# Performance work log

Measured on AMD Instinct MI355X. Metric: run time of the kernel, lower is better.

The kernel has to match this reference:

```python
import jax, jax.numpy as jnp
import numpy as np

N, E, F, H, G, C = 50000, 800000, 128, 64, 512, 10
RATIO = 0.5  # forward arg `ratio` baked as constant


def seg_mean(msgs, idx, n):
    s = jax.ops.segment_sum(msgs, idx, num_segments=n)
    cnt = jax.ops.segment_sum(jnp.ones(idx.shape[0], msgs.dtype), idx, num_segments=n)
    return s / jnp.maximum(cnt, 1.0)[:, None]


def sage(x, src, dst, Wl, bl, Wr, ew=None):
    # PyG SAGEConv: lin_l(mean_{j->i} msg_j) + lin_r(x_i); weighted variant scales messages
    m = x[src] if ew is None else x[src] * ew[:, None]
    agg = seg_mean(m, dst, x.shape[0])
    return agg @ Wl + bl + x @ Wr


def topk_mask(scores, seg, num_graphs, ratio):
    # per-graph (segment) top-k edge selection: keep ceil(ratio*edges_in_graph) highest scores
    e = scores.shape[0]
    counts = jax.ops.segment_sum(jnp.ones(e, jnp.float32), seg, num_segments=num_graphs)
    order = jnp.lexsort((-scores, seg))  # sort by segment, then score descending
    seg_sorted = seg[order]
    starts = jnp.concatenate([jnp.zeros(1, jnp.float32), jnp.cumsum(counts)[:-1]])
    rank = jnp.arange(e, dtype=jnp.float32) - starts[seg_sorted]
    k = jnp.ceil(ratio * counts)
    sel = (rank < k[seg_sorted]).astype(scores.dtype)
    return jnp.zeros(e, scores.dtype).at[order].set(sel)


def setup_inputs():
    key = jax.random.key(0)
    ks = jax.random.split(key, 16)
    w = lambda k, shape, fan: (jax.random.normal(k, shape, jnp.float32) / np.sqrt(fan))
    return {
        'x': jax.random.normal(ks[0], (N, F), jnp.float32),
        'edge_index': jax.random.randint(ks[1], (2, E), 0, N, jnp.int32),
        'batch': jnp.sort(jax.random.randint(ks[2], (N,), 0, G, jnp.int32)),
        'W1l': w(ks[3], (F, H), F), 'b1l': jnp.zeros(H, jnp.float32), 'W1r': w(ks[4], (F, H), F),
        'W2l': w(ks[5], (H, H), H), 'b2l': jnp.zeros(H, jnp.float32), 'W2r': w(ks[6], (H, H), H),
        'W3l': w(ks[7], (H, H), H), 'b3l': jnp.zeros(H, jnp.float32), 'W3r': w(ks[8], (H, H), H),
        'Wlin1': w(ks[9], (H, H), H), 'blin1': jnp.zeros(H, jnp.float32),
        'Wlin2': w(ks[10], (H, C), H), 'blin2': jnp.zeros(C, jnp.float32),
    }


def reference(x, edge_index, batch, W1l, b1l, W1r, W2l, b2l, W2r, W3l, b3l, W3r, Wlin1, blin1, Wlin2, blin2):
    src, dst = edge_index[0], edge_index[1]
    h = jax.nn.relu(sage(x, src, dst, W1l, b1l, W1r))
    edge_scores = jnp.sum(h[src] * h[dst], axis=-1)  # [E]
    seg = batch[src]  # graph id per edge (sections)
    sampled = topk_mask(edge_scores, seg, G, RATIO)
    ew = edge_scores * sampled
    h = jax.nn.relu(sage(h, src, dst, W2l, b2l, W2r, ew))
    h = jax.nn.relu(sage(h, src, dst, W3l, b3l, W3r, ew))
    pooled = seg_mean(h, batch, G)  # global_mean_pool
    z = jax.nn.relu(pooled @ Wlin1 + blin1)
    z = z @ Wlin2 + blin2  # dropout inactive in eval
    return jax.nn.log_softmax(z, axis=-1), sampled
```

## Files before the change

### kernel.cpp

```cpp
#include <hip/hip_runtime.h>
#include <hip/hip_bf16.h>
#include <math.h>

static constexpr int N = 50000;
static constexpr int E = 800000;
static constexpr int F = 128;
static constexpr int H = 64;
static constexpr int G = 512;
static constexpr int C = 10;
static constexpr int CAP = 256;
static constexpr int NWIN = 8;
static constexpr int EB = E / 256;
static constexpr int GB2 = (N + 31) / 32;
static constexpr int SB = E / 256;

static inline int cdiv(long a, int b) { return (int)((a + b - 1) / b); }

__device__ __forceinline__ float uinv_score(unsigned u) {
  return (u & 0x80000000u) ? __uint_as_float(u & 0x7fffffffu) : __uint_as_float(~u);
}

__device__ __forceinline__ int2 pack_slot(int s, int d, int g, int e) {
  unsigned a = (unsigned)s | ((unsigned)(d & 0x7FFF) << 17);
  unsigned b = ((unsigned)d >> 15) | ((unsigned)g << 2) | ((unsigned)e << 11);
  return make_int2((int)a, (int)b);
}
__device__ __forceinline__ int slot_src(int2 p) { return p.x & 0x1FFFF; }
__device__ __forceinline__ int slot_dst(int2 p) {
  return (int)(((unsigned)p.x >> 17) | (((unsigned)p.y & 3u) << 15));
}
__device__ __forceinline__ int slot_g(int2 p) { return (int)(((unsigned)p.y >> 2) & 0x1FFu); }
__device__ __forceinline__ int slot_eid(int2 p) { return (int)((unsigned)p.y >> 11); }

__global__ void k_deg_goff(const int* __restrict__ dst, const int* __restrict__ batch,
                           int* __restrict__ deg, int* __restrict__ goff) {
  for (int i = blockIdx.x * 256 + threadIdx.x; i < N; i += gridDim.x * 256) {
    int b = batch[i];
    if (i == 0) {
      for (int g = 0; g <= b; ++g) goff[g] = 0;
    } else {
      int p = batch[i - 1];
      for (int g = p + 1; g <= b; ++g) goff[g] = i;
    }
    if (i == N - 1) {
      for (int g = b + 1; g <= G; ++g) goff[g] = N;
    }
  }
  const int4* d4 = (const int4*)dst;
  for (int i = blockIdx.x * 256 + threadIdx.x; i < E / 4; i += gridDim.x * 256) {
    int4 v = d4[i];
    atomicAdd(&deg[v.x], 1);
    atomicAdd(&deg[v.y], 1);
    atomicAdd(&deg[v.z], 1);
    atomicAdd(&deg[v.w], 1);
  }
}

__global__ void k_scan_a(const int* __restrict__ cnt, int* __restrict__ off,
                         int* __restrict__ bsum, int n) {
  __shared__ int wsum[16];
  int tid = threadIdx.x, lane = tid & 63, wv = tid >> 6;
  int idx = blockIdx.x * 4096 + tid * 4;
  int v0 = (idx + 0 < n) ? cnt[idx + 0] : 0;
  int v1 = (idx + 1 < n) ? cnt[idx + 1] : 0;
  int v2 = (idx + 2 < n) ? cnt[idx + 2] : 0;
  int v3 = (idx + 3 < n) ? cnt[idx + 3] : 0;
  int local = v0 + v1 + v2 + v3;
  int inc = local;
  for (int d = 1; d < 64; d <<= 1) {
    int t = __shfl_up(inc, d);
    if (lane >= d) inc += t;
  }
  if (lane == 63) wsum[wv] = inc;
  __syncthreads();
  if (tid < 16) {
    int t = wsum[tid];
    for (int d = 1; d < 16; d <<= 1) {
      int u = __shfl_up(t, d);
      if (tid >= d) t += u;
    }
    wsum[tid] = t;
  }
  __syncthreads();
  int woff = (wv > 0) ? wsum[wv - 1] : 0;
  int excl = woff + inc - local;
  if (idx + 0 < n) off[idx + 0] = excl;
  if (idx + 1 < n) off[idx + 1] = excl + v0;
  if (idx + 2 < n) off[idx + 2] = excl + v0 + v1;
  if (idx + 3 < n) off[idx + 3] = excl + v0 + v1 + v2;
  if (tid == 0) bsum[blockIdx.x] = wsum[15];
}

__global__ void k_scan_c(int* __restrict__ off, int* __restrict__ cursor,
                         const int* __restrict__ bsum, int n, int nb) {
  __shared__ int spre[34];
  int tid = threadIdx.x;
  if (tid < 32) {
    int v = (tid < nb) ? bsum[tid] : 0;
    int inc = v;
    for (int d = 1; d < 32; d <<= 1) {
      int t = __shfl_up(inc, d);
      if (tid >= d) inc += t;
    }
    spre[tid] = inc - v;
  }
  __syncthreads();
  int i = blockIdx.x * 256 + tid;
  if (i < n) {
    int v = off[i] + spre[i >> 12];
    off[i] = v;
    cursor[i] = v;
  } else if (i == n) {
    off[n] = spre[nb];
  }
}

__global__ void k_fill_gemm(const int* __restrict__ src, const int* __restrict__ dst,
                            const int* __restrict__ batch, int* __restrict__ cursor,
                            int2* __restrict__ csrp, int* __restrict__ einv,
                            const float* __restrict__ x, const float* __restrict__ Wl,
                            const float* __restrict__ Wr, const float* __restrict__ bl,
                            float* __restrict__ y, float* __restrict__ r) {
  __shared__ float sx[16][F];
  int lane = threadIdx.x, ty = threadIdx.y;
  int bq = blockIdx.x / 9, br = blockIdx.x - bq * 9;
  if (br == 0) {
    int tid = ty * 64 + lane;
    int row0 = bq * 16;
    const float4* gsrc = (const float4*)(x + (size_t)row0 * F);
    float4* sdst = (float4*)(&sx[0][0]);
#pragma unroll
    for (int i = tid; i < 16 * F / 4; i += 256) sdst[i] = gsrc[i];
    __syncthreads();
    float al[4], ar[4];
    float bias = bl[lane];
#pragma unroll
    for (int j = 0; j < 4; ++j) { al[j] = 0.f; ar[j] = bias; }
#pragma unroll 4
    for (int f = 0; f < F; ++f) {
      float wl = Wl[f * H + lane];
      float wr = Wr[f * H + lane];
#pragma unroll
      for (int j = 0; j < 4; ++j) {
        float xv = sx[ty * 4 + j][f];
        al[j] += xv * wl;
        ar[j] += xv * wr;
      }
    }
#pragma unroll
    for (int j = 0; j < 4; ++j) {
      int row = row0 + ty * 4 + j;
      y[(size_t)row * H + lane] = al[j];
      r[(size_t)row * H + lane] = ar[j];
    }
  } else {
    int tid = ty * 64 + lane;
    int fid = bq * 8 + (br - 1);
    int win = fid / EB;
    int blk = fid - win * EB;
    int e = blk * 256 + tid;
    int d = dst[e];
    int lo = win * (N / NWIN), hi = lo + (N / NWIN);
    if (d < lo || d >= hi) return;
    int s = src[e];
    int g = batch[s];
    int slot = atomicAdd(&cursor[d], 1);
    csrp[slot] = pack_slot(s, d, g, e);
    einv[e] = slot;
  }
}

template <int K>
__global__ void k_gemm2h(const float* __restrict__ in, const float* __restrict__ Wl,
                         const float* __restrict__ Wr, const float* __restrict__ b,
                         __hip_bfloat16* __restrict__ y, float* __restrict__ r) {
  __shared__ float sx[16][K];
  int lane = threadIdx.x, ty = threadIdx.y;
  int tid = ty * 64 + lane;
  int row0 = blockIdx.x * 16;
  const float4* gsrc = (const float4*)(in + (size_t)row0 * K);
  float4* sdst = (float4*)(&sx[0][0]);
#pragma unroll
  for (int i = tid; i < 16 * K / 4; i += 256) sdst[i] = gsrc[i];
  __syncthreads();
  float al[4], ar[4];
  float bias = b[lane];
#pragma unroll
  for (int j = 0; j < 4; ++j) { al[j] = 0.f; ar[j] = bias; }
#pragma unroll 4
  for (int f = 0; f < K; ++f) {
    float wl = Wl[f * H + lane];
    float wr = Wr[f * H + lane];
#pragma unroll
    for (int j = 0; j < 4; ++j) {
      float xv = sx[ty * 4 + j][f];
      al[j] += xv * wl;
      ar[j] += xv * wr;
    }
  }
#pragma unroll
  for (int j = 0; j < 4; ++j) {
    int row = row0 + ty * 4 + j;
    y[(size_t)row * H + lane] = __float2bfloat16(al[j]);
    r[(size_t)row * H + lane] = ar[j];
  }
}

__global__ void k_agg1(const float* __restrict__ y, const float* __restrict__ r,
                       const int2* __restrict__ csrp, const int* __restrict__ off,
                       float* __restrict__ out) {
  int node = blockIdx.x * 8 + threadIdx.y;
  int lane = threadIdx.x;
  int q = lane >> 3, c = lane & 7;
  int s0 = off[node], s1 = off[node + 1];
  float4 a0 = make_float4(0.f, 0.f, 0.f, 0.f);
  float4 a1 = make_float4(0.f, 0.f, 0.f, 0.f);
  int i = s0 + q;
  for (; i + 8 < s1; i += 16) {
    int se0 = slot_src(csrp[i]);
    int se1 = slot_src(csrp[i + 8]);
    const float4* p0 = (const float4*)(y + (size_t)se0 * H);
    const float4* p1 = (const float4*)(y + (size_t)se1 * H);
    float4 u0 = p0[c], v0 = p0[c + 8];
    float4 u1 = p1[c], v1 = p1[c + 8];
    a0.x += u0.x + u1.x; a0.y += u0.y + u1.y; a0.z += u0.z + u1.z; a0.w += u0.w + u1.w;
    a1.x += v0.x + v1.x; a1.y += v0.y + v1.y; a1.z += v0.z + v1.z; a1.w += v0.w + v1.w;
  }
  for (; i < s1; i += 8) {
    int se = slot_src(csrp[i]);
    const float4* p = (const float4*)(y + (size_t)se * H);
    float4 u = p[c], v = p[c + 8];
    a0.x += u.x; a0.y += u.y; a0.z += u.z; a0.w += u.w;
    a1.x += v.x; a1.y += v.y; a1.z += v.z; a1.w += v.w;
  }
#pragma unroll
  for (int d = 8; d < 64; d <<= 1) {
    a0.x += __shfl_xor(a0.x, d); a0.y += __shfl_xor(a0.y, d);
    a0.z += __shfl_xor(a0.z, d); a0.w += __shfl_xor(a0.w, d);
    a1.x += __shfl_xor(a1.x, d); a1.y += __shfl_xor(a1.y, d);
    a1.z += __shfl_xor(a1.z, d); a1.w += __shfl_xor(a1.w, d);
  }
  if (q == 0) {
    float inv = 1.f / fmaxf((float)(s1 - s0), 1.f);
    const float4* rp = (const float4*)(r + (size_t)node * H);
    float4 r0 = rp[c], r1 = rp[c + 8];
    float4 o0, o1;
    o0.x = fmaxf(a0.x * inv + r0.x, 0.f); o0.y = fmaxf(a0.y * inv + r0.y, 0.f);
    o0.z = fmaxf(a0.z * inv + r0.z, 0.f); o0.w = fmaxf(a0.w * inv + r0.w, 0.f);
    o1.x = fmaxf(a1.x * inv + r1.x, 0.f); o1.y = fmaxf(a1.y * inv + r1.y, 0.f);
    o1.z = fmaxf(a1.z * inv + r1.z, 0.f); o1.w = fmaxf(a1.w * inv + r1.w, 0.f);
    float4* op = (float4*)(out + (size_t)node * H);
    op[c] = o0; op[c + 8] = o1;
  }
}

__global__ void k_agg_w(const __hip_bfloat16* __restrict__ y, const float* __restrict__ r,
                        const int2* __restrict__ csr2, const int* __restrict__ cnt2,
                        const int* __restrict__ off, float* __restrict__ out) {
  int node = blockIdx.x * 8 + threadIdx.y;
  int lane = threadIdx.x;
  int q = lane >> 3, c = lane & 7;
  int b0 = off[node], cn = cnt2[node];
  float a[8] = {0.f, 0.f, 0.f, 0.f, 0.f, 0.f, 0.f, 0.f};
  for (int j = q; j < cn; j += 8) {
    int2 sw = csr2[b0 + j];
    float w = __int_as_float(sw.y);
    uint4 pk = ((const uint4*)((const unsigned short*)y + (size_t)sw.x * H))[c];
    a[0] += w * __uint_as_float(pk.x << 16); a[1] += w * __uint_as_float(pk.x & 0xffff0000u);
    a[2] += w * __uint_as_float(pk.y << 16); a[3] += w * __uint_as_float(pk.y & 0xffff0000u);
    a[4] += w * __uint_as_float(pk.z << 16); a[5] += w * __uint_as_float(pk.z & 0xffff0000u);
    a[6] += w * __uint_as_float(pk.w << 16); a[7] += w * __uint_as_float(pk.w & 0xffff0000u);
  }
#pragma unroll
  for (int d = 8; d < 64; d <<= 1) {
#pragma unroll
    for (int j = 0; j < 8; ++j) a[j] += __shfl_xor(a[j], d);
  }
  if (q == 0) {
    int degn = off[node + 1] - off[node];
    float inv = 1.f / fmaxf((float)degn, 1.f);
    const float4* rp = (const float4*)(r + (size_t)node * H);
    float4 r0 = rp[2 * c], r1 = rp[2 * c + 1];
    float4 o0, o1;
    o0.x = fmaxf(a[0] * inv + r0.x, 0.f); o0.y = fmaxf(a[1] * inv + r0.y, 0.f);
    o0.z = fmaxf(a[2] * inv + r0.z, 0.f); o0.w = fmaxf(a[3] * inv + r0.w, 0.f);
    o1.x = fmaxf(a[4] * inv + r1.x, 0.f); o1.y = fmaxf(a[5] * inv + r1.y, 0.f);
    o1.z = fmaxf(a[6] * inv + r1.z, 0.f); o1.w = fmaxf(a[7] * inv + r1.w, 0.f);
    float4* op = (float4*)(out + (size_t)node * H);
    op[2 * c] = o0; op[2 * c + 1] = o1;
  }
}

__global__ void k_score_g2h(const float* __restrict__ h1, const int2* __restrict__ csrp,
                            unsigned* __restrict__ scoreu_csr,
                            unsigned short* __restrict__ seg_csr, int* __restrict__ hist,
                            const float* __restrict__ Wl, const float* __restrict__ Wr,
                            const float* __restrict__ bl,
                            __hip_bfloat16* __restrict__ y, float* __restrict__ r) {
  __shared__ float sx[32][H];
  int lane = threadIdx.x, ty = threadIdx.y;
  int q3 = blockIdx.x / 3, r3 = blockIdx.x - q3 * 3;
  if (r3 == 0 && q3 < GB2) {
    int tid = ty * 64 + lane;
    int row0 = q3 * 32;
    {
      int row = row0 + (tid >> 4);
      if (row < N)
        ((float4*)(&sx[0][0]))[tid] = ((const float4*)h1)[(size_t)row * (H / 4) + (tid & 15)];
    }
    __syncthreads();
    float al[4], ar[4];
    float bias = bl[lane];
#pragma unroll
    for (int j = 0; j < 4; ++j) { al[j] = 0.f; ar[j] = bias; }
#pragma unroll 4
    for (int f = 0; f < H; ++f) {
      float wl = Wl[f * H + lane];
      float wr = Wr[f * H + lane];
#pragma unroll
      for (int j = 0; j < 4; ++j) {
        float xv = sx[ty * 4 + j][f];
        al[j] += xv * wl;
        ar[j] += xv * wr;
      }
    }
#pragma unroll
    for (int j = 0; j < 4; ++j) {
      int row = row0 + ty * 4 + j;
      if (row < N) {
        y[(size_t)row * H + lane] = __float2bfloat16(al[j]);
        r[(size_t)row * H + lane] = ar[j];
      }
    }
  } else {
    int sid = blockIdx.x - (q3 + (r3 > 0 ? 1 : 0));
    int q = lane >> 4, c = lane & 15;
    int s = (sid * 8 + ty) * 32 + q * 8;
    int2 se[8];
#pragma unroll
    for (int j = 0; j < 8; ++j) se[j] = csrp[s + j];
    float4 xr[8], yr[8];
#pragma unroll
    for (int j = 0; j < 8; ++j)
      xr[j] = ((const float4*)(h1 + (size_t)slot_src(se[j]) * H))[c];
#pragma unroll
    for (int j = 0; j < 8; ++j)
      yr[j] = ((const float4*)(h1 + (size_t)slot_dst(se[j]) * H))[c];
    float p[8];
#pragma unroll
    for (int j = 0; j < 8; ++j)
      p[j] = yr[j].x * xr[j].x + yr[j].y * xr[j].y + yr[j].z * xr[j].z + yr[j].w * xr[j].w;
#pragma unroll
    for (int d = 1; d < 16; d <<= 1) {
#pragma unroll
      for (int j = 0; j < 8; ++j) p[j] += __shfl_xor(p[j], d);
    }
    if (c == 0) {
#pragma unroll
      for (int j = 0; j < 8; ++j) {
        int g = slot_g(se[j]);
        unsigned u = __float_as_uint(p[j]);
        u = (u & 0x80000000u) ? ~u : (u | 0x80000000u);
        scoreu_csr[s + j] = u;
        seg_csr[s + j] = (unsigned short)g;
        atomicAdd(&hist[g * 256 + (int)(u >> 24)], 1);
      }
    }
  }
}

__global__ void k_hist(const unsigned* __restrict__ scoreu, const unsigned short* __restrict__ seg,
                       const unsigned* __restrict__ prefix, int* __restrict__ hist, int pass) {
  int e = (blockIdx.x * 256 + threadIdx.x) * 4;
  if (e >= E) return;
  uint4 u4 = *(const uint4*)(scoreu + e);
  ushort4 s4 = *(const ushort4*)(seg + e);
  unsigned uu[4] = {u4.x, u4.y, u4.z, u4.w};
  int gg[4] = {(int)s4.x, (int)s4.y, (int)s4.z, (int)s4.w};
  int predshift = 32 - 8 * pass;
  int bshift = 24 - 8 * pass;
#pragma unroll
  for (int j = 0; j < 4; ++j) {
    unsigned u = uu[j];
    int g = gg[j];
    if ((u >> predshift) == (prefix[g] >> predshift))
      atomicAdd(&hist[g * 256 + (int)((u >> bshift) & 0xFFu)], 1);
  }
}

__global__ void k_scan(int* __restrict__ hist, unsigned* __restrict__ prefix,
                       int* __restrict__ krem, int pass) {
  int g = blockIdx.x;
  int lane = threadIdx.x;
  int4* row = (int4*)(hist + (size_t)g * 256);
  int4 v = row[lane];
  int vj[4] = {v.x, v.y, v.z, v.w};
  int s = v.x + v.y + v.z + v.w;
  int inc = s;
  for (int d = 1; d < 64; d <<= 1) {
    int t = __shfl_up(inc, d);
    if (lane >= d) inc += t;
  }
  int T = __shfl(inc, 63);
  int k = (pass == 0) ? ((T + 1) >> 1) : krem[g];
  int excl = inc - s;
  int pre[4] = {excl, excl + vj[0], excl + vj[0] + vj[1], excl + vj[0] + vj[1] + vj[2]};
  int bsel_l = -1, newk_l = 0;
  if (k > 0) {
    for (int j = 3; j >= 0; --j) {
      int suf = T - pre[j];
      if (suf >= k) { bsel_l = 4 * lane + j; newk_l = k - (suf - vj[j]); break; }
    }
  }
  unsigned long long mask = __ballot(bsel_l >= 0);
  int bsel = 255, newk = 0;
  if (k > 0 && mask) {
    int hi = 63 - __builtin_clzll(mask);
    bsel = __shfl(bsel_l, hi);
    newk = __shfl(newk_l, hi);
  }
  if (lane == 0) {
    unsigned base = (pass == 0) ? 0u : prefix[g];
    prefix[g] = base | ((unsigned)bsel << (24 - 8 * pass));
    krem[g] = newk;
  }
  row[lane] = make_int4(0, 0, 0, 0);
}

__global__ void k_select(const unsigned* __restrict__ scoreu_csr,
                         const unsigned short* __restrict__ seg_csr,
                         const unsigned* __restrict__ thresh,
                         int* __restrict__ eqcnt, int* __restrict__ eqlist,
                         unsigned char* __restrict__ sel_csr, float* __restrict__ ew_csr) {
  int s = (blockIdx.x * 256 + threadIdx.x) * 4;
  if (s >= E) return;
  uint4 u4 = *(const uint4*)(scoreu_csr + s);
  ushort4 g4 = *(const ushort4*)(seg_csr + s);
  unsigned uu[4] = {u4.x, u4.y, u4.z, u4.w};
  int gg[4] = {(int)g4.x, (int)g4.y, (int)g4.z, (int)g4.w};
  float ew[4];
  unsigned char sl[4];
#pragma unroll
  for (int j = 0; j < 4; ++j) {
    unsigned u = uu[j];
    int g = gg[j];
    unsigned t = thresh[g];
    unsigned um = u & 0xffffff00u;
    float sel = 0.f;
    if (um > t) sel = 1.f;
    else if (um == t) {
      int slot = atomicAdd(&eqcnt[g], 1);
      if (slot < CAP) eqlist[g * CAP + slot] = s + j;
    }
    sl[j] = (unsigned char)sel;
    ew[j] = uinv_score(u) * sel;
  }
  *(uchar4*)(sel_csr + s) = make_uchar4(sl[0], sl[1], sl[2], sl[3]);
  *(float4*)(ew_csr + s) = make_float4(ew[0], ew[1], ew[2], ew[3]);
}

__global__ void k_resolve(const int* __restrict__ krem, const int* __restrict__ eqcnt,
                          const int* __restrict__ eqlist, const int2* __restrict__ csrp,
                          const unsigned* __restrict__ scoreu_csr,
                          unsigned char* __restrict__ sel_csr, float* __restrict__ ew_csr) {
  int g = blockIdx.x * 256 + threadIdx.x;
  if (g >= G) return;
  int c = eqcnt[g]; if (c > CAP) c = CAP;
  int r = krem[g];  if (r > c) r = c;
  const int* lst = eqlist + g * CAP;
  unsigned last_u = 0u; int last_e = -1; bool first = true;
  for (int i = 0; i < r; ++i) {
    unsigned bu = 0u; int be = -1, bs = -1;
    for (int j = 0; j < c; ++j) {
      int slot = lst[j];
      unsigned u = scoreu_csr[slot];
      int eid = slot_eid(csrp[slot]);
      bool after = first || (u < last_u) || (u == last_u && eid > last_e);
      if (after && (bs < 0 || u > bu || (u == bu && eid < be))) { bu = u; be = eid; bs = slot; }
    }
    if (bs < 0) break;
    sel_csr[bs] = 1;
    ew_csr[bs] = uinv_score(bu);
    last_u = bu; last_e = be; first = false;
  }
}

__global__ void k_samp_comp(const unsigned char* __restrict__ sel,
                            const int2* __restrict__ csrp, const float* __restrict__ ewc,
                            const int* __restrict__ off, int2* __restrict__ csr2,
                            int* __restrict__ cnt2,
                            const int* __restrict__ einv, float* __restrict__ sampled) {
  int lane = threadIdx.x, ty = threadIdx.y;
  if (blockIdx.x < N / 8) {
    int node = blockIdx.x * 8 + ty;
    int s0 = off[node], s1 = off[node + 1];
    unsigned long long lt = ((unsigned long long)1 << lane) - 1;
    int cum = 0;
    for (int i0 = s0; i0 < s1; i0 += 64) {
      int i = i0 + lane;
      bool f = (i < s1) && sel[i];
      unsigned long long m = __ballot(f);
      if (f) {
        int rank = __popcll(m & lt);
        csr2[s0 + cum + rank] = make_int2(slot_src(csrp[i]), __float_as_int(ewc[i]));
      }
      cum += __popcll(m);
    }
    if (lane == 0) cnt2[node] = cum;
  } else {
    int tid = ty * 64 + lane;
    int e = ((blockIdx.x - N / 8) * 512 + tid) * 4;
    if (e >= E) return;
    int4 iv = *(const int4*)(einv + e);
    float4 o;
    o.x = (float)sel[iv.x];
    o.y = (float)sel[iv.y];
    o.z = (float)sel[iv.z];
    o.w = (float)sel[iv.w];
    *(float4*)(sampled + e) = o;
  }
}

__global__ void k_poolhead(const float* __restrict__ h3, const int* __restrict__ goff,
                           const float* __restrict__ W1, const float* __restrict__ b1,
                           const float* __restrict__ W2, const float* __restrict__ b2,
                           float* __restrict__ outp) {
  int g = blockIdx.x;
  int tid = threadIdx.x;
  int h = tid & 63, j = tid >> 6;
  int s0 = goff[g], s1 = goff[g + 1];
  float a = 0.f;
  for (int n = s0 + j; n < s1; n += 8) a += h3[(size_t)n * H + h];
  __shared__ float sp[8][H];
  __shared__ float p[H], z1[H], z2[C];
  __shared__ float lse;
  sp[j][h] = a;
  __syncthreads();
  if (j == 0) {
    float s = sp[0][h] + sp[1][h] + sp[2][h] + sp[3][h]
            + sp[4][h] + sp[5][h] + sp[6][h] + sp[7][h];
    float inv = 1.f / fmaxf((float)(s1 - s0), 1.f);
    p[h] = s * inv;
  }
  __syncthreads();
  if (j == 0) {
    float acc = b1[h];
#pragma unroll 8
    for (int f = 0; f < H; ++f) acc += p[f] * W1[f * H + h];
    z1[h] = fmaxf(acc, 0.f);
  }
  __syncthreads();
  if (tid < C) {
    float a2 = b2[tid];
#pragma unroll 8
    for (int f = 0; f < H; ++f) a2 += z1[f] * W2[f * C + tid];
    z2[tid] = a2;
  }
  __syncthreads();
  if (tid == 0) {
    float m = z2[0];
    for (int c = 1; c < C; ++c) m = fmaxf(m, z2[c]);
    float s = 0.f;
    for (int c = 0; c < C; ++c) s += expf(z2[c] - m);
    lse = m + logf(s);
  }
  __syncthreads();
  if (tid < C) outp[(size_t)g * C + tid] = z2[tid] - lse;
}

extern "C" void kernel_launch(void* const* d_in, const int* in_sizes, int n_in,
                              void* d_out, int out_size, void* d_ws, size_t ws_size,
                              hipStream_t stream) {
  const float* x     = (const float*)d_in[0];
  const int*   ei    = (const int*)d_in[1];
  const int*   batch = (const int*)d_in[2];
  const float* W1l   = (const float*)d_in[3];
  const float* b1l   = (const float*)d_in[4];
  const float* W1r   = (const float*)d_in[5];
  const float* W2l   = (const float*)d_in[6];
  const float* b2l   = (const float*)d_in[7];
  const float* W2r   = (const float*)d_in[8];
  const float* W3l   = (const float*)d_in[9];
  const float* b3l   = (const float*)d_in[10];
  const float* W3r   = (const float*)d_in[11];
  const float* Wlin1 = (const float*)d_in[12];
  const float* blin1 = (const float*)d_in[13];
  const float* Wlin2 = (const float*)d_in[14];
  const float* blin2 = (const float*)d_in[15];

  const int* srcv = ei;
  const int* dstv = ei + E;

  float* out_ls   = (float*)d_out;
  float* out_samp = out_ls + G * C;

  char* w = (char*)d_ws;
  auto carve = [&](size_t bytes) { void* p = (void*)w; w += (bytes + 255) & ~(size_t)255; return p; };
  char* zbase   = w;
  int*      deg     = (int*)carve((size_t)N * 4);
  int*      eqcnt   = (int*)carve((size_t)G * 4);
  int*      hist    = (int*)carve((size_t)G * 256 * 4);
  size_t    zbytes  = (size_t)(w - zbase);
  float*    h1      = (float*)carve((size_t)N * H * 4);
  float*    h2      = (float*)carve((size_t)N * H * 4);
  float*    h3      = (float*)carve((size_t)N * H * 4);
  float*    yb      = (float*)carve((size_t)N * H * 4);
  float*    rb      = (float*)carve((size_t)N * H * 4);
  __hip_bfloat16* ybh = (__hip_bfloat16*)carve((size_t)N * H * 2);
  unsigned* scoreu_csr = (unsigned*)carve((size_t)E * 4);
  unsigned short* seg_csr = (unsigned short*)carve((size_t)E * 2);
  float*    ew_csr     = (float*)carve((size_t)E * 4);
  unsigned char* sel_csr = (unsigned char*)carve((size_t)E);
  int2*     csrp    = (int2*)carve((size_t)E * 8);
  int*      einv    = (int*)carve((size_t)E * 4);
  int*      off     = (int*)carve((size_t)(N + 1) * 4);
  int*      cursor  = (int*)carve((size_t)N * 4);
  int*      cnt2    = (int*)carve((size_t)N * 4);
  int*      goff    = (int*)carve((size_t)(G + 1) * 4);
  unsigned* prefix  = (unsigned*)carve((size_t)G * 4);
  int*      krem    = (int*)carve((size_t)G * 4);
  int*      eqlist  = (int*)carve((size_t)G * CAP * 4);
  int*      bsum    = (int*)carve((size_t)16 * 4);
  int2*     csr2    = (int2*)carve((size_t)E * 8);

  hipMemsetAsync(zbase, 0, zbytes, stream);

  k_deg_goff<<<256, 256, 0, stream>>>(dstv, batch, deg, goff);
  int nb = cdiv(N, 4096);
  k_scan_a<<<nb, 1024, 0, stream>>>(deg, off, bsum, N);
  k_scan_c<<<cdiv(N + 1, 256), 256, 0, stream>>>(off, cursor, bsum, N, nb);

  k_fill_gemm<<<9 * EB, dim3(64, 4), 0, stream>>>(srcv, dstv, batch, cursor, csrp, einv,
                                                  x, W1l, W1r, b1l, yb, rb);

  k_agg1<<<N / 8, dim3(64, 8), 0, stream>>>(yb, rb, csrp, off, h1);

  k_score_g2h<<<SB + GB2, dim3(64, 8), 0, stream>>>(h1, csrp, scoreu_csr, seg_csr, hist,
                                                    W2l, W2r, b2l, ybh, rb);
  k_scan<<<G, 64, 0, stream>>>(hist, prefix, krem, 0);
  for (int p = 1; p <= 2; ++p) {
    k_hist<<<cdiv(E / 4, 256), 256, 0, stream>>>(scoreu_csr, seg_csr, prefix, hist, p);
    k_scan<<<G, 64, 0, stream>>>(hist, prefix, krem, p);
  }
  k_select<<<cdiv(E / 4, 256), 256, 0, stream>>>(scoreu_csr, seg_csr, prefix,
                                                 eqcnt, eqlist, sel_csr, ew_csr);
  k_resolve<<<cdiv(G, 256), 256, 0, stream>>>(krem, eqcnt, eqlist, csrp, scoreu_csr,
                                              sel_csr, ew_csr);

  k_samp_comp<<<N / 8 + cdiv(E / 4, 512), dim3(64, 8), 0, stream>>>(
      sel_csr, csrp, ew_csr, off, csr2, cnt2, einv, out_samp);

  k_agg_w<<<N / 8, dim3(64, 8), 0, stream>>>(ybh, rb, csr2, cnt2, off, h2);

  k_gemm2h<H><<<N / 16, dim3(64, 4), 0, stream>>>(h2, W3l, W3r, b3l, ybh, rb);
  k_agg_w<<<N / 8, dim3(64, 8), 0, stream>>>(ybh, rb, csr2, cnt2, off, h3);

  k_poolhead<<<G, 512, 0, stream>>>(h3, goff, Wlin1, blin1, Wlin2, blin2, out_ls);
}
```

Baseline: 424.0 us.

## Move layer-1 GEMM into degree kernel and batch CSR fill per window

The first-layer dense projection moves out of the CSR fill kernel and into the degree/graph-offset kernel as extra blocks, so it overlaps the atomic degree counting instead of the fill phase. The fill kernel becomes standalone. Each block now handles a 1280-edge chunk for one destination window and preloads the dst values into registers before the atomic slot assignment. This cuts the block count and the scheduling overhead of the old 9-way interleaved launch, but the GEMM blocks now compete with the degree atomics, and the larger per-block work may reduce parallelism. Two shuffle statements are also swapped, which has no effect.

```diff
diff --git a/kernel.cpp b/kernel.cpp
--- a/kernel.cpp
+++ b/kernel.cpp
@@ -10,7 +10,9 @@
 static constexpr int C = 10;
 static constexpr int CAP = 256;
 static constexpr int NWIN = 8;
-static constexpr int EB = E / 256;
+static constexpr int FILL_CH = 1280;
+static constexpr int FB = E / FILL_CH;
+static constexpr int DEGB = 256;
 static constexpr int GB2 = (N + 31) / 32;
 static constexpr int SB = E / 256;
 
@@ -32,9 +34,45 @@
 __device__ __forceinline__ int slot_g(int2 p) { return (int)(((unsigned)p.y >> 2) & 0x1FFu); }
 __device__ __forceinline__ int slot_eid(int2 p) { return (int)((unsigned)p.y >> 11); }
 
-__global__ void k_deg_goff(const int* __restrict__ dst, const int* __restrict__ batch,
-                           int* __restrict__ deg, int* __restrict__ goff) {
-  for (int i = blockIdx.x * 256 + threadIdx.x; i < N; i += gridDim.x * 256) {
+__global__ void k_deg_gemm(const int* __restrict__ dst, const int* __restrict__ batch,
+                           int* __restrict__ deg, int* __restrict__ goff,
+                           const float* __restrict__ x, const float* __restrict__ Wl,
+                           const float* __restrict__ Wr, const float* __restrict__ bl,
+                           float* __restrict__ y, float* __restrict__ r) {
+  __shared__ float sx[16][F];
+  int lane = threadIdx.x, ty = threadIdx.y;
+  int tid = ty * 64 + lane;
+  if (blockIdx.x >= DEGB) {
+    int row0 = (blockIdx.x - DEGB) * 16;
+    const float4* gsrc = (const float4*)(x + (size_t)row0 * F);
+    float4* sdst = (float4*)(&sx[0][0]);
+#pragma unroll
+    for (int i = tid; i < 16 * F / 4; i += 256) sdst[i] = gsrc[i];
+    __syncthreads();
+    float al[4], ar[4];
+    float bias = bl[lane];
+#pragma unroll
+    for (int j = 0; j < 4; ++j) { al[j] = 0.f; ar[j] = bias; }
+#pragma unroll 4
+    for (int f = 0; f < F; ++f) {
+      float wl = Wl[f * H + lane];
+      float wr = Wr[f * H + lane];
+#pragma unroll
+      for (int j = 0; j < 4; ++j) {
+        float xv = sx[ty * 4 + j][f];
+        al[j] += xv * wl;
+        ar[j] += xv * wr;
+      }
+    }
+#pragma unroll
+    for (int j = 0; j < 4; ++j) {
+      int row = row0 + ty * 4 + j;
+      y[(size_t)row * H + lane] = al[j];
+      r[(size_t)row * H + lane] = ar[j];
+    }
+    return;
+  }
+  for (int i = blockIdx.x * 256 + tid; i < N; i += DEGB * 256) {
     int b = batch[i];
     if (i == 0) {
       for (int g = 0; g <= b; ++g) goff[g] = 0;
@@ -47,7 +85,7 @@
     }
   }
   const int4* d4 = (const int4*)dst;
-  for (int i = blockIdx.x * 256 + threadIdx.x; i < E / 4; i += gridDim.x * 256) {
+  for (int i = blockIdx.x * 256 + tid; i < E / 4; i += DEGB * 256) {
     int4 v = d4[i];
     atomicAdd(&deg[v.x], 1);
     atomicAdd(&deg[v.y], 1);
@@ -115,58 +153,27 @@
   }
 }
 
-__global__ void k_fill_gemm(const int* __restrict__ src, const int* __restrict__ dst,
-                            const int* __restrict__ batch, int* __restrict__ cursor,
-                            int2* __restrict__ csrp, int* __restrict__ einv,
-                            const float* __restrict__ x, const float* __restrict__ Wl,
-                            const float* __restrict__ Wr, const float* __restrict__ bl,
-                            float* __restrict__ y, float* __restrict__ r) {
-  __shared__ float sx[16][F];
-  int lane = threadIdx.x, ty = threadIdx.y;
-  int bq = blockIdx.x / 9, br = blockIdx.x - bq * 9;
-  if (br == 0) {
-    int tid = ty * 64 + lane;
-    int row0 = bq * 16;
-    const float4* gsrc = (const float4*)(x + (size_t)row0 * F);
-    float4* sdst = (float4*)(&sx[0][0]);
-#pragma unroll
-    for (int i = tid; i < 16 * F / 4; i += 256) sdst[i] = gsrc[i];
-    __syncthreads();
-    float al[4], ar[4];
-    float bias = bl[lane];
-#pragma unroll
-    for (int j = 0; j < 4; ++j) { al[j] = 0.f; ar[j] = bias; }
-#pragma unroll 4
-    for (int f = 0; f < F; ++f) {
-      float wl = Wl[f * H + lane];
-      float wr = Wr[f * H + lane];
-#pragma unroll
-      for (int j = 0; j < 4; ++j) {
-        float xv = sx[ty * 4 + j][f];
-        al[j] += xv * wl;
-        ar[j] += xv * wr;
-      }
-    }
-#pragma unroll
-    for (int j = 0; j < 4; ++j) {
-      int row = row0 + ty * 4 + j;
-      y[(size_t)row * H + lane] = al[j];
-      r[(size_t)row * H + lane] = ar[j];
-    }
-  } else {
-    int tid = ty * 64 + lane;
-    int fid = bq * 8 + (br - 1);
-    int win = fid / EB;
-    int blk = fid - win * EB;
-    int e = blk * 256 + tid;
-    int d = dst[e];
-    int lo = win * (N / NWIN), hi = lo + (N / NWIN);
-    if (d < lo || d >= hi) return;
-    int s = src[e];
-    int g = batch[s];
-    int slot = atomicAdd(&cursor[d], 1);
-    csrp[slot] = pack_slot(s, d, g, e);
-    einv[e] = slot;
+__global__ void k_fill(const int* __restrict__ src, const int* __restrict__ dst,
+                       const int* __restrict__ batch, int* __restrict__ cursor,
+                       int2* __restrict__ csrp, int* __restrict__ einv) {
+  int win = blockIdx.x & 7;
+  int chunk = blockIdx.x >> 3;
+  int lo = win * (N / NWIN), hi = lo + (N / NWIN);
+  int base = chunk * FILL_CH + threadIdx.x;
+  int dd[FILL_CH / 256];
+#pragma unroll
+  for (int it = 0; it < FILL_CH / 256; ++it) dd[it] = dst[base + it * 256];
+#pragma unroll
+  for (int it = 0; it < FILL_CH / 256; ++it) {
+    int d = dd[it];
+    if (d >= lo && d < hi) {
+      int e = base + it * 256;
+      int s = src[e];
+      int g = batch[s];
+      int slot = atomicAdd(&cursor[d], 1);
+      csrp[slot] = pack_slot(s, d, g, e);
+      einv[e] = slot;
+    }
   }
 }
 
@@ -238,7 +245,7 @@
     a0.x += __shfl_xor(a0.x, d); a0.y += __shfl_xor(a0.y, d);
     a0.z += __shfl_xor(a0.z, d); a0.w += __shfl_xor(a0.w, d);
     a1.x += __shfl_xor(a1.x, d); a1.y += __shfl_xor(a1.y, d);
-    a1.z += __shfl_xor(a1.z, d); a1.w += __shfl_xor(a1.w, d);
+    a1.w += __shfl_xor(a1.w, d); a1.z += __shfl_xor(a1.z, d);
   }
   if (q == 0) {
     float inv = 1.f / fmaxf((float)(s1 - s0), 1.f);
@@ -625,13 +632,13 @@
 
   hipMemsetAsync(zbase, 0, zbytes, stream);
 
-  k_deg_goff<<<256, 256, 0, stream>>>(dstv, batch, deg, goff);
+  k_deg_gemm<<<DEGB + N / 16, dim3(64, 4), 0, stream>>>(dstv, batch, deg, goff,
+                                                        x, W1l, W1r, b1l, yb, rb);
   int nb = cdiv(N, 4096);
   k_scan_a<<<nb, 1024, 0, stream>>>(deg, off, bsum, N);
   k_scan_c<<<cdiv(N + 1, 256), 256, 0, stream>>>(off, cursor, bsum, N, nb);
 
-  k_fill_gemm<<<9 * EB, dim3(64, 4), 0, stream>>>(srcv, dstv, batch, cursor, csrp, einv,
-                                                  x, W1l, W1r, b1l, yb, rb);
+  k_fill<<<8 * FB, 256, 0, stream>>>(srcv, dstv, batch, cursor, csrp, einv);
 
   k_agg1<<<N / 8, dim3(64, 8), 0, stream>>>(yb, rb, csrp, off, h1);
 
```

New measurement: 436.9 us. 1.03x slower.

## Reuse degree-count atomic return values as CSR ranks to avoid second atomic pass

Applied to the files above, without the earlier changes.

The return value of the degree-counting atomicAdd is stored as a per-edge 16-bit rank. The CSR fill then computes each slot as off[dst]+rank with no atomics. This removes the 8-window filtered fill pass and the cursor array, and each fill thread now handles four edges with vectorised loads. The cost is an extra E*2-byte buffer written and read. Ordering within a row still depends on atomic order, and ranks are truncated to 16 bits, which assumes node in-degree stays below 65536.

```diff
diff --git a/kernel.cpp b/kernel.cpp
--- a/kernel.cpp
+++ b/kernel.cpp
@@ -9,8 +9,8 @@
 static constexpr int G = 512;
 static constexpr int C = 10;
 static constexpr int CAP = 256;
-static constexpr int NWIN = 8;
-static constexpr int EB = E / 256;
+static constexpr int NFB = (E / 4 + 255) / 256;
+static constexpr int GB1 = N / 16;
 static constexpr int GB2 = (N + 31) / 32;
 static constexpr int SB = E / 256;
 
@@ -33,8 +33,10 @@
 __device__ __forceinline__ int slot_eid(int2 p) { return (int)((unsigned)p.y >> 11); }
 
 __global__ void k_deg_goff(const int* __restrict__ dst, const int* __restrict__ batch,
-                           int* __restrict__ deg, int* __restrict__ goff) {
-  for (int i = blockIdx.x * 256 + threadIdx.x; i < N; i += gridDim.x * 256) {
+                           int* __restrict__ deg, int* __restrict__ goff,
+                           unsigned short* __restrict__ rank16) {
+  int tid = threadIdx.x;
+  for (int i = blockIdx.x * 256 + tid; i < N; i += gridDim.x * 256) {
     int b = batch[i];
     if (i == 0) {
       for (int g = 0; g <= b; ++g) goff[g] = 0;
@@ -47,12 +49,14 @@
     }
   }
   const int4* d4 = (const int4*)dst;
-  for (int i = blockIdx.x * 256 + threadIdx.x; i < E / 4; i += gridDim.x * 256) {
+  for (int i = blockIdx.x * 256 + tid; i < E / 4; i += gridDim.x * 256) {
     int4 v = d4[i];
-    atomicAdd(&deg[v.x], 1);
-    atomicAdd(&deg[v.y], 1);
-    atomicAdd(&deg[v.z], 1);
-    atomicAdd(&deg[v.w], 1);
+    ushort4 rk;
+    rk.x = (unsigned short)atomicAdd(&deg[v.x], 1);
+    rk.y = (unsigned short)atomicAdd(&deg[v.y], 1);
+    rk.z = (unsigned short)atomicAdd(&deg[v.z], 1);
+    rk.w = (unsigned short)atomicAdd(&deg[v.w], 1);
+    *(ushort4*)(rank16 + (size_t)i * 4) = rk;
   }
 }
 
@@ -91,8 +95,7 @@
   if (tid == 0) bsum[blockIdx.x] = wsum[15];
 }
 
-__global__ void k_scan_c(int* __restrict__ off, int* __restrict__ cursor,
-                         const int* __restrict__ bsum, int n, int nb) {
+__global__ void k_scan_c(int* __restrict__ off, const int* __restrict__ bsum, int n, int nb) {
   __shared__ int spre[34];
   int tid = threadIdx.x;
   if (tid < 32) {
@@ -107,66 +110,73 @@
   __syncthreads();
   int i = blockIdx.x * 256 + tid;
   if (i < n) {
-    int v = off[i] + spre[i >> 12];
-    off[i] = v;
-    cursor[i] = v;
+    off[i] = off[i] + spre[i >> 12];
   } else if (i == n) {
     off[n] = spre[nb];
   }
 }
 
 __global__ void k_fill_gemm(const int* __restrict__ src, const int* __restrict__ dst,
-                            const int* __restrict__ batch, int* __restrict__ cursor,
+                            const unsigned short* __restrict__ rank16,
+                            const int* __restrict__ batch, const int* __restrict__ off,
                             int2* __restrict__ csrp, int* __restrict__ einv,
                             const float* __restrict__ x, const float* __restrict__ Wl,
                             const float* __restrict__ Wr, const float* __restrict__ bl,
                             float* __restrict__ y, float* __restrict__ r) {
   __shared__ float sx[16][F];
   int lane = threadIdx.x, ty = threadIdx.y;
-  int bq = blockIdx.x / 9, br = blockIdx.x - bq * 9;
+  int tid = ty * 64 + lane;
+  int bq = blockIdx.x / 5, br = blockIdx.x - bq * 5;
   if (br == 0) {
-    int tid = ty * 64 + lane;
-    int row0 = bq * 16;
-    const float4* gsrc = (const float4*)(x + (size_t)row0 * F);
-    float4* sdst = (float4*)(&sx[0][0]);
-#pragma unroll
-    for (int i = tid; i < 16 * F / 4; i += 256) sdst[i] = gsrc[i];
-    __syncthreads();
-    float al[4], ar[4];
-    float bias = bl[lane];
-#pragma unroll
-    for (int j = 0; j < 4; ++j) { al[j] = 0.f; ar[j] = bias; }
+    int i = bq * 256 + tid;
+    if (i < E / 4) {
+      int4 dv = ((const int4*)dst)[i];
+      int4 sv = ((const int4*)src)[i];
+      ushort4 rv = *(const ushort4*)(rank16 + (size_t)i * 4);
+      int dd[4] = {dv.x, dv.y, dv.z, dv.w};
+      int ss[4] = {sv.x, sv.y, sv.z, sv.w};
+      int rr[4] = {rv.x, rv.y, rv.z, rv.w};
+      int e0 = i * 4;
+      int slots[4];
+#pragma unroll
+      for (int j = 0; j < 4; ++j) {
+        int g = batch[ss[j]];
+        int slot = off[dd[j]] + rr[j];
+        csrp[slot] = pack_slot(ss[j], dd[j], g, e0 + j);
+        slots[j] = slot;
+      }
+      *(int4*)(einv + e0) = make_int4(slots[0], slots[1], slots[2], slots[3]);
+    }
+    return;
+  }
+  int gid = bq * 4 + (br - 1);
+  if (gid >= GB1) return;
+  int row0 = gid * 16;
+  const float4* gsrc = (const float4*)(x + (size_t)row0 * F);
+  float4* sdst = (float4*)(&sx[0][0]);
+#pragma unroll
+  for (int i = tid; i < 16 * F / 4; i += 256) sdst[i] = gsrc[i];
+  __syncthreads();
+  float al[4], ar[4];
+  float bias = bl[lane];
+#pragma unroll
+  for (int j = 0; j < 4; ++j) { al[j] = 0.f; ar[j] = bias; }
 #pragma unroll 4
-    for (int f = 0; f < F; ++f) {
-      float wl = Wl[f * H + lane];
-      float wr = Wr[f * H + lane];
-#pragma unroll
-      for (int j = 0; j < 4; ++j) {
-        float xv = sx[ty * 4 + j][f];
-        al[j] += xv * wl;
-        ar[j] += xv * wr;
-      }
-    }
+  for (int f = 0; f < F; ++f) {
+    float wl = Wl[f * H + lane];
+    float wr = Wr[f * H + lane];
 #pragma unroll
     for (int j = 0; j < 4; ++j) {
-      int row = row0 + ty * 4 + j;
-      y[(size_t)row * H + lane] = al[j];
-      r[(size_t)row * H + lane] = ar[j];
-    }
-  } else {
-    int tid = ty * 64 + lane;
-    int fid = bq * 8 + (br - 1);
-    int win = fid / EB;
-    int blk = fid - win * EB;
-    int e = blk * 256 + tid;
-    int d = dst[e];
-    int lo = win * (N / NWIN), hi = lo + (N / NWIN);
-    if (d < lo || d >= hi) return;
-    int s = src[e];
-    int g = batch[s];
-    int slot = atomicAdd(&cursor[d], 1);
-    csrp[slot] = pack_slot(s, d, g, e);
-    einv[e] = slot;
+      float xv = sx[ty * 4 + j][f];
+      al[j] += xv * wl;
+      ar[j] += xv * wr;
+    }
+  }
+#pragma unroll
+  for (int j = 0; j < 4; ++j) {
+    int row = row0 + ty * 4 + j;
+    y[(size_t)row * H + lane] = al[j];
+    r[(size_t)row * H + lane] = ar[j];
   }
 }
 
@@ -613,8 +623,8 @@
   unsigned char* sel_csr = (unsigned char*)carve((size_t)E);
   int2*     csrp    = (int2*)carve((size_t)E * 8);
   int*      einv    = (int*)carve((size_t)E * 4);
+  unsigned short* rank16 = (unsigned short*)carve((size_t)E * 2);
   int*      off     = (int*)carve((size_t)(N + 1) * 4);
-  int*      cursor  = (int*)carve((size_t)N * 4);
   int*      cnt2    = (int*)carve((size_t)N * 4);
   int*      goff    = (int*)carve((size_t)(G + 1) * 4);
   unsigned* prefix  = (unsigned*)carve((size_t)G * 4);
@@ -625,13 +635,14 @@
 
   hipMemsetAsync(zbase, 0, zbytes, stream);
 
-  k_deg_goff<<<256, 256, 0, stream>>>(dstv, batch, deg, goff);
+  k_deg_goff<<<256, 256, 0, stream>>>(dstv, batch, deg, goff, rank16);
   int nb = cdiv(N, 4096);
   k_scan_a<<<nb, 1024, 0, stream>>>(deg, off, bsum, N);
-  k_scan_c<<<cdiv(N + 1, 256), 256, 0, stream>>>(off, cursor, bsum, N, nb);
-
-  k_fill_gemm<<<9 * EB, dim3(64, 4), 0, stream>>>(srcv, dstv, batch, cursor, csrp, einv,
-                                                  x, W1l, W1r, b1l, yb, rb);
+  k_scan_c<<<cdiv(N + 1, 256), 256, 0, stream>>>(off, bsum, N, nb);
+
+  k_fill_gemm<<<5 * NFB, dim3(64, 4), 0, stream>>>(srcv, dstv, rank16, batch, off,
+                                                   csrp, einv,
+                                                   x, W1l, W1r, b1l, yb, rb);
 
   k_agg1<<<N / 8, dim3(64, 8), 0, stream>>>(yb, rb, csrp, off, h1);
 
```

After: 405.4 us. 1.05x faster.
